# Kernel tuning notes

Measured on AMD Instinct MI355X. Metric: run time of the kernel, lower is better.

Reference implementation:

```python
import jax, jax.numpy as jnp
import numpy as np

B, NS, NQ = 128, 128, 512
D_IN, D_OUT = 256, 64


def setup_inputs() -> dict:
    key = jax.random.key(0)
    ks = jax.random.split(key, 6)
    return {
        "phi_support": jax.random.normal(ks[0], (B, NS, D_IN), dtype=jnp.float32),
        "y_support": jax.random.normal(ks[1], (B, NS, D_OUT), dtype=jnp.float32),
        "phi_query": jax.random.normal(ks[2], (B, NQ, D_IN), dtype=jnp.float32),
        "y_query": jax.random.normal(ks[3], (B, NQ, D_OUT), dtype=jnp.float32),
        # xavier-uniform-ish params
        "m_prior": jax.random.uniform(ks[4], (D_IN, D_OUT), minval=-1.0, maxval=1.0) * np.sqrt(6.0 / (D_IN + D_OUT)),
        "S_inv_prior_asym": jax.random.uniform(ks[5], (D_IN, D_IN), minval=-1.0, maxval=1.0) * np.sqrt(6.0 / (2 * D_IN)),
        "sig_eps": jnp.array([0.1], dtype=jnp.float32),
    }


def reference(phi_support, y_support, phi_query, y_query, m_prior, S_inv_prior_asym, sig_eps):
    alpha = 1.0
    d_out = m_prior.shape[1]
    # prior precision (symmetric PSD by construction) and natural-param prior mean
    S_inv_prior = alpha * (S_inv_prior_asym @ S_inv_prior_asym.T)          # [D_in, D_in]
    m_prior_nat = S_inv_prior @ m_prior                                     # [D_in, D_out]
    # posterior precision / covariance per task (nobs > 0 branch)
    S_inv = jnp.einsum('bni,bnj->bij', phi_support, phi_support) + S_inv_prior  # [B, D_in, D_in]
    S = jnp.linalg.inv(S_inv)                                               # batched small inverse
    rhs = jnp.einsum('bni,bnk->bik', phi_support, y_support) + m_prior_nat  # [B, D_in, D_out]
    m = S @ rhs                                                             # [B, D_in, D_out]
    # predictive mean and spread
    mu = phi_query @ m                                                      # [B, Q, D_out]
    spread_fac = 1.0 + jnp.einsum('bqi,bij,bqj->bq', phi_query, S, phi_query)  # [B, Q]
    # sig = spread_fac (x) (eye * sig_eps) : diagonal [B, Q, D_out, D_out]
    diag = jnp.eye(d_out, dtype=mu.dtype) * sig_eps                         # [D_out, D_out]
    sig = spread_fac[..., None, None] * diag
    # nll: logdet of diagonal sig + quadratic form with its inverse (diag -> reciprocal)
    logdet = d_out * (jnp.log(spread_fac) + jnp.log(sig_eps))               # [B, Q]
    resid = y_query - mu
    quadf = jnp.sum(resid * resid, axis=-1) / (spread_fac * sig_eps)        # [B, Q]
    nll = logdet.mean() + quadf.mean()
    return mu, sig, nll
```

## Files before the change

kernel.cpp:

```cpp
#include <hip/hip_runtime.h>
#include <math.h>

#define B_T   128
#define NS    128
#define NQ    512
#define DIN   256
#define DOUT  64

#define MU_SIZE  (B_T*NQ*DOUT)
#define SIG_SIZE (B_T*NQ*DOUT*DOUT)
#define NLL_IDX  (MU_SIZE + SIG_SIZE)

__global__ __launch_bounds__(256) void k_prior_sp(const float* __restrict__ A,
                                                  double* __restrict__ Sp) {
    __shared__ float Ai[16][260];
    __shared__ float Aj[16][260];
    int bi = blockIdx.x;
    int i0 = (bi >> 4) << 4;
    int j0 = (bi & 15) << 4;
    int tid = threadIdx.x;
    for (int idx = tid; idx < 16 * 256; idx += 256) {
        int r = idx >> 8, c = idx & 255;
        Ai[r][c] = A[(i0 + r) * 256 + c];
        Aj[r][c] = A[(j0 + r) * 256 + c];
    }
    __syncthreads();
    int r = tid >> 4, c = tid & 15;
    double acc = 0.0;
    for (int k = 0; k < 256; ++k)
        acc += (double)Ai[r][k] * (double)Aj[c][k];
    Sp[(i0 + r) * 256 + (j0 + c)] = acc;
}

__global__ __launch_bounds__(64) void k_prior_mpn(const double* __restrict__ Sp,
                                                  const float* __restrict__ MP,
                                                  double* __restrict__ MPN) {
    int i = blockIdx.x, k = threadIdx.x;
    double acc = 0.0;
    for (int t = 0; t < 256; ++t)
        acc += Sp[i * 256 + t] * (double)MP[t * 64 + k];
    MPN[i * 64 + k] = acc;
}

__global__ __launch_bounds__(256) void k_build_G(const float* __restrict__ PHI,
                                                 const double* __restrict__ Sp,
                                                 double* __restrict__ G) {
    __shared__ float As[128][64];
    __shared__ float Bs[128][64];
    int b = blockIdx.x;
    int by = blockIdx.y;
    int ti = 0;
    while (((ti + 1) * (ti + 2)) / 2 <= by) ti++;
    int tj = by - (ti * (ti + 1)) / 2;
    int i0 = ti * 64, j0 = tj * 64;
    int tid = threadIdx.x;
    const float* Pb = PHI + b * (NS * DIN);
    for (int idx = tid; idx < 128 * 64; idx += 256) {
        int n = idx >> 6, c = idx & 63;
        As[n][c] = Pb[n * 256 + i0 + c];
        Bs[n][c] = Pb[n * 256 + j0 + c];
    }
    __syncthreads();
    int tx = tid & 15, ty = tid >> 4;
    double acc[4][4];
#pragma unroll
    for (int r = 0; r < 4; ++r)
#pragma unroll
        for (int s = 0; s < 4; ++s) acc[r][s] = 0.0;
    for (int n = 0; n < 128; ++n) {
        float a0 = As[n][4 * ty + 0], a1 = As[n][4 * ty + 1];
        float a2 = As[n][4 * ty + 2], a3 = As[n][4 * ty + 3];
        float b0 = Bs[n][4 * tx + 0], b1 = Bs[n][4 * tx + 1];
        float b2 = Bs[n][4 * tx + 2], b3 = Bs[n][4 * tx + 3];
        acc[0][0] += (double)a0 * b0; acc[0][1] += (double)a0 * b1;
        acc[0][2] += (double)a0 * b2; acc[0][3] += (double)a0 * b3;
        acc[1][0] += (double)a1 * b0; acc[1][1] += (double)a1 * b1;
        acc[1][2] += (double)a1 * b2; acc[1][3] += (double)a1 * b3;
        acc[2][0] += (double)a2 * b0; acc[2][1] += (double)a2 * b1;
        acc[2][2] += (double)a2 * b2; acc[2][3] += (double)a2 * b3;
        acc[3][0] += (double)a3 * b0; acc[3][1] += (double)a3 * b1;
        acc[3][2] += (double)a3 * b2; acc[3][3] += (double)a3 * b3;
    }
    double* Gb = G + b * 65536;
#pragma unroll
    for (int r = 0; r < 4; ++r) {
        int i = i0 + 4 * ty + r;
#pragma unroll
        for (int s = 0; s < 4; ++s) {
            int j = j0 + 4 * tx + s;
            Gb[i * 256 + j] = acc[r][s] + Sp[i * 256 + j];
        }
    }
}

__global__ __launch_bounds__(256) void k_build_rhs(const float* __restrict__ PHI,
                                                   const float* __restrict__ Y,
                                                   const double* __restrict__ MPN,
                                                   double* __restrict__ RHS) {
    __shared__ float As[128][64];
    __shared__ float Ys[128][64];
    int b = blockIdx.x, i0 = blockIdx.y * 64, tid = threadIdx.x;
    const float* Pb = PHI + b * (NS * DIN);
    const float* Yb = Y + b * (NS * DOUT);
    for (int idx = tid; idx < 128 * 64; idx += 256) {
        int n = idx >> 6, c = idx & 63;
        As[n][c] = Pb[n * 256 + i0 + c];
        Ys[n][c] = Yb[n * 64 + c];
    }
    __syncthreads();
    int tx = tid & 15, ty = tid >> 4;
    double acc[4][4];
#pragma unroll
    for (int r = 0; r < 4; ++r)
#pragma unroll
        for (int s = 0; s < 4; ++s) acc[r][s] = 0.0;
    for (int n = 0; n < 128; ++n) {
        float a0 = As[n][4 * ty + 0], a1 = As[n][4 * ty + 1];
        float a2 = As[n][4 * ty + 2], a3 = As[n][4 * ty + 3];
        float y0 = Ys[n][4 * tx + 0], y1 = Ys[n][4 * tx + 1];
        float y2 = Ys[n][4 * tx + 2], y3 = Ys[n][4 * tx + 3];
        acc[0][0] += (double)a0 * y0; acc[0][1] += (double)a0 * y1;
        acc[0][2] += (double)a0 * y2; acc[0][3] += (double)a0 * y3;
        acc[1][0] += (double)a1 * y0; acc[1][1] += (double)a1 * y1;
        acc[1][2] += (double)a1 * y2; acc[1][3] += (double)a1 * y3;
        acc[2][0] += (double)a2 * y0; acc[2][1] += (double)a2 * y1;
        acc[2][2] += (double)a2 * y2; acc[2][3] += (double)a2 * y3;
        acc[3][0] += (double)a3 * y0; acc[3][1] += (double)a3 * y1;
        acc[3][2] += (double)a3 * y2; acc[3][3] += (double)a3 * y3;
    }
    double* Rb = RHS + b * 16384;
#pragma unroll
    for (int r = 0; r < 4; ++r) {
        int i = i0 + 4 * ty + r;
#pragma unroll
        for (int s = 0; s < 4; ++s) {
            int kc = 4 * tx + s;
            Rb[i * 64 + kc] = acc[r][s] + MPN[i * 64 + kc];
        }
    }
}

__global__ __launch_bounds__(256) void k_chol(double* __restrict__ G,
                                              double* __restrict__ LT,
                                              double* __restrict__ INVD) {
    __shared__ double P[8][256];
    int b = blockIdx.x, tid = threadIdx.x;
    double* Gb = G + b * 65536;
    double* LTb = LT + b * 65536;
    for (int k0 = 0; k0 < 256; k0 += 8) {
#pragma unroll
        for (int p = 0; p < 8; ++p) P[p][tid] = Gb[tid * 256 + k0 + p];
        __syncthreads();
        for (int p = 0; p < 8; ++p) {
            int k = k0 + p;
            if (tid >= k) {
                double v = P[p][tid];
                for (int p2 = 0; p2 < p; ++p2) v -= P[p2][tid] * P[p2][k];
                P[p][tid] = v;
            }
            __syncthreads();
            double d = sqrt(fmax(P[p][k], 1e-300));
            double inv = 1.0 / d;
            if (tid > k) P[p][tid] *= inv;
            else if (tid == k) { P[p][tid] = d; INVD[b * 256 + k] = inv; }
            __syncthreads();
        }
#pragma unroll
        for (int p = 0; p < 8; ++p) {
            int k = k0 + p;
            if (tid >= k) LTb[k * 256 + tid] = P[p][tid];
        }
        int ty = tid >> 4, tx = tid & 15;
        for (int i = k0 + 8 + ty; i < 256; i += 16) {
            double pi[8];
#pragma unroll
            for (int p = 0; p < 8; ++p) pi[p] = P[p][i];
            for (int j = k0 + 8 + tx; j <= i; j += 16) {
                double g = Gb[i * 256 + j];
#pragma unroll
                for (int p = 0; p < 8; ++p) g -= pi[p] * P[p][j];
                Gb[i * 256 + j] = g;
            }
        }
        __syncthreads();
    }
}

__global__ __launch_bounds__(256) void k_trinv(const double* __restrict__ LT,
                                               double* __restrict__ TI,
                                               float* __restrict__ TIF) {
    __shared__ double SHD[8192];
    int b = blockIdx.x, tid = threadIdx.x;
    const double* LTb = LT + b * 65536;
    double* TIb = TI + b * 65536;
    float* TIFb = TIF + b * 65536;
    for (int idx = tid; idx < 65536; idx += 256) {
        int i = idx >> 8, k = idx & 255;
        if (k > i) { TIb[idx] = 0.0; TIFb[idx] = 0.0f; }
    }
    for (int idx = tid; idx < 8192; idx += 256) {
        int g = idx >> 10, rem = idx & 1023, k = rem >> 5, i = rem & 31;
        SHD[idx] = LTb[(32 * g + k) * 256 + 32 * g + i];
    }
    __syncthreads();
    {
        int g = tid >> 5, j = tid & 31;
        const double* D = SHD + g * 1024;
        double x[32];
#pragma unroll
        for (int i = 0; i < 32; ++i) {
            double s = (i == j) ? 1.0 : 0.0;
#pragma unroll
            for (int k = 0; k < i; ++k) {
                double lv = D[k * 32 + i];
                s -= (k >= j) ? lv * x[k] : 0.0;
            }
            double inv = 1.0 / D[i * 32 + i];
            x[i] = (i >= j) ? s * inv : 0.0;
        }
#pragma unroll
        for (int i = 0; i < 32; ++i) {
            int gi = 32 * g + i, gj = 32 * g + j;
            TIb[gi * 256 + gj] = x[i];
            TIFb[gi * 256 + gj] = (float)x[i];
        }
    }
    __syncthreads();
    double* Bsh = SHD;
    int j = tid & 31, ig = tid >> 5;
    for (int I = 1; I < 8; ++I) {
        for (int J = I - 1; J >= 0; --J) {
            double acc[4] = {0.0, 0.0, 0.0, 0.0};
            for (int K = J; K < I; ++K) {
                for (int kk = 0; kk < 32; ++kk) {
                    double tv = TIb[(32 * K + kk) * 256 + 32 * J + j];
#pragma unroll
                    for (int r = 0; r < 4; ++r) {
                        double lv = LTb[(32 * K + kk) * 256 + 32 * I + ig * 4 + r];
                        acc[r] += lv * tv;
                    }
                }
            }
            __syncthreads();
#pragma unroll
            for (int r = 0; r < 4; ++r) Bsh[(ig * 4 + r) * 32 + j] = acc[r];
            __syncthreads();
            double c[4] = {0.0, 0.0, 0.0, 0.0};
            for (int k = 0; k < 32; ++k) {
                double bv = Bsh[k * 32 + j];
#pragma unroll
                for (int r = 0; r < 4; ++r) {
                    double dv = TIb[(32 * I + ig * 4 + r) * 256 + 32 * I + k];
                    c[r] -= dv * bv;
                }
            }
#pragma unroll
            for (int r = 0; r < 4; ++r) {
                int gi = 32 * I + ig * 4 + r, gj = 32 * J + j;
                TIb[gi * 256 + gj] = c[r];
                TIFb[gi * 256 + gj] = (float)c[r];
            }
        }
        __syncthreads();
    }
}

__global__ __launch_bounds__(256) void k_gemm_Z(const double* __restrict__ TI,
                                                const double* __restrict__ RHS,
                                                double* __restrict__ Z) {
    __shared__ double As[32][64];
    __shared__ double Bs[64][64];
    int b = blockIdx.x, i0 = blockIdx.y * 32;
    int tid = threadIdx.x, c = tid & 63, rg = tid >> 6;
    const double* TIb = TI + b * 65536;
    const double* Rb = RHS + b * 16384;
    double* Zb = Z + b * 16384;
    double acc[8] = {};
    for (int k0 = 0; k0 <= i0; k0 += 64) {
        for (int idx = tid; idx < 2048; idx += 256) {
            int r = idx >> 6, kk = idx & 63;
            As[r][kk] = TIb[(i0 + r) * 256 + k0 + kk];
        }
        for (int idx = tid; idx < 4096; idx += 256) {
            int kk = idx >> 6, cc = idx & 63;
            Bs[kk][cc] = Rb[(k0 + kk) * 64 + cc];
        }
        __syncthreads();
        for (int kk = 0; kk < 64; ++kk) {
            double bv = Bs[kk][c];
#pragma unroll
            for (int r = 0; r < 8; ++r)
                acc[r] += As[rg * 8 + r][kk] * bv;
        }
        __syncthreads();
    }
#pragma unroll
    for (int r = 0; r < 8; ++r)
        Zb[(i0 + rg * 8 + r) * 64 + c] = acc[r];
}

__global__ __launch_bounds__(256) void k_gemm_M(const double* __restrict__ TI,
                                                const double* __restrict__ Z,
                                                double* __restrict__ M) {
    __shared__ double As[64][32];
    __shared__ double Bs[64][64];
    int b = blockIdx.x, i0 = blockIdx.y * 32;
    int tid = threadIdx.x, c = tid & 63, rg = tid >> 6;
    const double* TIb = TI + b * 65536;
    const double* Zb = Z + b * 16384;
    double* Mb = M + b * 16384;
    double acc[8] = {};
    for (int k0 = (i0 >> 6) << 6; k0 < 256; k0 += 64) {
        for (int idx = tid; idx < 2048; idx += 256) {
            int kk = idx >> 5, ri = idx & 31;
            As[kk][ri] = TIb[(k0 + kk) * 256 + i0 + ri];
        }
        for (int idx = tid; idx < 4096; idx += 256) {
            int kk = idx >> 6, cc = idx & 63;
            Bs[kk][cc] = Zb[(k0 + kk) * 64 + cc];
        }
        __syncthreads();
        for (int kk = 0; kk < 64; ++kk) {
            double bv = Bs[kk][c];
#pragma unroll
            for (int r = 0; r < 8; ++r)
                acc[r] += As[kk][rg * 8 + r] * bv;
        }
        __syncthreads();
    }
#pragma unroll
    for (int r = 0; r < 8; ++r)
        Mb[(i0 + rg * 8 + r) * 64 + c] = acc[r];
}

__global__ __launch_bounds__(256) void k_spread_gemm(const float* __restrict__ PHIQ,
                                                     const float* __restrict__ TIF,
                                                     float* __restrict__ PSUM) {
    __shared__ float Qs[64][65];
    __shared__ float Ts[64][65];
    int b = blockIdx.x, q0 = blockIdx.y * 64, I = blockIdx.z, i0 = I * 64;
    int tid = threadIdx.x, tx = tid & 15, ty = tid >> 4;
    const float* Qb = PHIQ + b * (NQ * DIN) + q0 * DIN;
    const float* Tb = TIF + b * 65536;
    float acc[4][4];
#pragma unroll
    for (int r = 0; r < 4; ++r)
#pragma unroll
        for (int s = 0; s < 4; ++s) acc[r][s] = 0.0f;
    for (int k0 = 0; k0 <= i0; k0 += 64) {
        for (int idx = tid; idx < 4096; idx += 256) {
            int r = idx >> 6, c = idx & 63;
            Qs[r][c] = Qb[r * 256 + k0 + c];
            Ts[c][r] = Tb[(i0 + r) * 256 + k0 + c];
        }
        __syncthreads();
        for (int kk = 0; kk < 64; ++kk) {
            float a0 = Qs[4 * ty + 0][kk], a1 = Qs[4 * ty + 1][kk];
            float a2 = Qs[4 * ty + 2][kk], a3 = Qs[4 * ty + 3][kk];
            float b0 = Ts[kk][4 * tx + 0], b1 = Ts[kk][4 * tx + 1];
            float b2 = Ts[kk][4 * tx + 2], b3 = Ts[kk][4 * tx + 3];
            acc[0][0] += a0 * b0; acc[0][1] += a0 * b1; acc[0][2] += a0 * b2; acc[0][3] += a0 * b3;
            acc[1][0] += a1 * b0; acc[1][1] += a1 * b1; acc[1][2] += a1 * b2; acc[1][3] += a1 * b3;
            acc[2][0] += a2 * b0; acc[2][1] += a2 * b1; acc[2][2] += a2 * b2; acc[2][3] += a2 * b3;
            acc[3][0] += a3 * b0; acc[3][1] += a3 * b1; acc[3][2] += a3 * b2; acc[3][3] += a3 * b3;
        }
        __syncthreads();
    }
#pragma unroll
    for (int r = 0; r < 4; ++r) {
        float p = acc[r][0] * acc[r][0] + acc[r][1] * acc[r][1]
                + acc[r][2] * acc[r][2] + acc[r][3] * acc[r][3];
        p += __shfl_down(p, 8, 16);
        p += __shfl_down(p, 4, 16);
        p += __shfl_down(p, 2, 16);
        p += __shfl_down(p, 1, 16);
        if (tx == 0) PSUM[(size_t)(b * 4 + I) * 512 + q0 + 4 * ty + r] = p;
    }
}

__global__ __launch_bounds__(256) void k_spread_combine(const float* __restrict__ PSUM,
                                                        float* __restrict__ SPREAD) {
    int b = blockIdx.x;
    for (int q = threadIdx.x; q < 512; q += 256) {
        float s = 1.0f;
#pragma unroll
        for (int I = 0; I < 4; ++I) s += PSUM[(size_t)(b * 4 + I) * 512 + q];
        SPREAD[b * 512 + q] = s;
    }
}

__global__ __launch_bounds__(256) void k_mu(const float* __restrict__ PHIQ,
                                            const double* __restrict__ M,
                                            float* __restrict__ MU) {
    __shared__ float Qs[64][65];
    __shared__ float Ms[64][64];
    int b = blockIdx.x, q0 = blockIdx.y * 64, tid = threadIdx.x;
    int tx = tid & 15, ty = tid >> 4;
    const float* Qb = PHIQ + b * (NQ * DIN) + q0 * DIN;
    const double* Mb = M + b * 16384;
    float acc[4][4];
#pragma unroll
    for (int r = 0; r < 4; ++r)
#pragma unroll
        for (int s = 0; s < 4; ++s) acc[r][s] = 0.0f;
    for (int c0 = 0; c0 < 256; c0 += 64) {
        for (int idx = tid; idx < 4096; idx += 256) {
            int r = idx >> 6, c = idx & 63;
            Qs[r][c] = Qb[r * 256 + c0 + c];
            Ms[r][c] = (float)Mb[(c0 + r) * 64 + c];
        }
        __syncthreads();
        for (int kk = 0; kk < 64; ++kk) {
            float a0 = Qs[4 * ty + 0][kk], a1 = Qs[4 * ty + 1][kk];
            float a2 = Qs[4 * ty + 2][kk], a3 = Qs[4 * ty + 3][kk];
            float b0 = Ms[kk][4 * tx + 0], b1 = Ms[kk][4 * tx + 1];
            float b2 = Ms[kk][4 * tx + 2], b3 = Ms[kk][4 * tx + 3];
            acc[0][0] += a0 * b0; acc[0][1] += a0 * b1; acc[0][2] += a0 * b2; acc[0][3] += a0 * b3;
            acc[1][0] += a1 * b0; acc[1][1] += a1 * b1; acc[1][2] += a1 * b2; acc[1][3] += a1 * b3;
            acc[2][0] += a2 * b0; acc[2][1] += a2 * b1; acc[2][2] += a2 * b2; acc[2][3] += a2 * b3;
            acc[3][0] += a3 * b0; acc[3][1] += a3 * b1; acc[3][2] += a3 * b2; acc[3][3] += a3 * b3;
        }
        __syncthreads();
    }
#pragma unroll
    for (int r = 0; r < 4; ++r) {
        float4 v = make_float4(acc[r][0], acc[r][1], acc[r][2], acc[r][3]);
        *(float4*)&MU[(b * NQ + q0 + 4 * ty + r) * 64 + 4 * tx] = v;
    }
}

__global__ __launch_bounds__(256) void k_nll_part(const float* __restrict__ YQ,
                                                  const float* __restrict__ MU,
                                                  const float* __restrict__ SPREAD,
                                                  const float* __restrict__ SE,
                                                  double* __restrict__ NLLP) {
    __shared__ double red[256];
    int tid = threadIdx.x;
    int bq = blockIdx.x * 256 + tid;
    float se = SE[0];
    float sp = SPREAD[bq];
    float qs = 0.0f;
    const float4* y4 = (const float4*)(YQ + bq * 64);
    const float4* m4 = (const float4*)(MU + bq * 64);
#pragma unroll
    for (int t = 0; t < 16; ++t) {
        float4 y = y4[t], m = m4[t];
        float dx = y.x - m.x, dy = y.y - m.y, dz = y.z - m.z, dw = y.w - m.w;
        qs += dx * dx + dy * dy + dz * dz + dw * dw;
    }
    float val = 64.0f * (logf(sp) + logf(se)) + qs / (sp * se);
    red[tid] = (double)val;
    __syncthreads();
    for (int s = 128; s > 0; s >>= 1) {
        if (tid < s) red[tid] += red[tid + s];
        __syncthreads();
    }
    if (tid == 0) NLLP[blockIdx.x] = red[0] * (1.0 / 65536.0);
}

__global__ __launch_bounds__(256) void k_nll_final(const double* __restrict__ NLLP,
                                                   float* __restrict__ out) {
    __shared__ double red[256];
    int tid = threadIdx.x;
    red[tid] = NLLP[tid];
    __syncthreads();
    for (int s = 128; s > 0; s >>= 1) {
        if (tid < s) red[tid] += red[tid + s];
        __syncthreads();
    }
    if (tid == 0) out[NLL_IDX] = (float)red[0];
}

__global__ __launch_bounds__(256) void k_sig(const float* __restrict__ SPREAD,
                                             const float* __restrict__ SE,
                                             float* __restrict__ out) {
    __shared__ float sv_s;
    int bq = blockIdx.x, tid = threadIdx.x;
    if (tid == 0) sv_s = SPREAD[bq] * SE[0];
    __syncthreads();
    float sv = sv_s;
    float* base = out + (size_t)MU_SIZE + (size_t)bq * 4096;
    int i = tid >> 2;
    int jb = (tid & 3) << 4;
    int d = i - jb;
    float vals[16];
#pragma unroll
    for (int t = 0; t < 16; ++t) vals[t] = (t == d) ? sv : 0.0f;
    float4* p = (float4*)(base + tid * 16);
    p[0] = make_float4(vals[0], vals[1], vals[2], vals[3]);
    p[1] = make_float4(vals[4], vals[5], vals[6], vals[7]);
    p[2] = make_float4(vals[8], vals[9], vals[10], vals[11]);
    p[3] = make_float4(vals[12], vals[13], vals[14], vals[15]);
}

extern "C" void kernel_launch(void* const* d_in, const int* in_sizes, int n_in,
                              void* d_out, int out_size, void* d_ws, size_t ws_size,
                              hipStream_t stream) {
    const float* PHI_S = (const float*)d_in[0];
    const float* Y_S   = (const float*)d_in[1];
    const float* PHI_Q = (const float*)d_in[2];
    const float* Y_Q   = (const float*)d_in[3];
    const float* MP    = (const float*)d_in[4];
    const float* AP    = (const float*)d_in[5];
    const float* SE    = (const float*)d_in[6];
    float* out = (float*)d_out;

    double* scratch = (double*)(out + MU_SIZE);
    double* G    = scratch;
    double* LT   = G + 8388608;
    double* RHS  = LT + 8388608;
    double* Z    = RHS + 2097152;
    double* TI   = Z + 2097152;
    double* Spd  = TI + 8388608;
    double* MPN  = Spd + 65536;
    double* INVD = MPN + 16384;
    float*  TIF  = (float*)(INVD + 32768);
    float*  PSUM = TIF + 8388608;
    float*  SPREAD = (float*)d_ws;
    double* NLLP   = (double*)((char*)d_ws + 65536 * 4);

    k_prior_sp      <<<256, 256, 0, stream>>>(AP, Spd);
    k_prior_mpn     <<<256, 64, 0, stream>>>(Spd, MP, MPN);
    k_build_G       <<<dim3(B_T, 10), 256, 0, stream>>>(PHI_S, Spd, G);
    k_build_rhs     <<<dim3(B_T, 4), 256, 0, stream>>>(PHI_S, Y_S, MPN, RHS);
    k_chol          <<<B_T, 256, 0, stream>>>(G, LT, INVD);
    k_trinv         <<<B_T, 256, 0, stream>>>(LT, TI, TIF);
    k_gemm_Z        <<<dim3(B_T, 8), 256, 0, stream>>>(TI, RHS, Z);
    k_gemm_M        <<<dim3(B_T, 8), 256, 0, stream>>>(TI, Z, RHS);
    k_spread_gemm   <<<dim3(B_T, 8, 4), 256, 0, stream>>>(PHI_Q, TIF, PSUM);
    k_spread_combine<<<B_T, 256, 0, stream>>>(PSUM, SPREAD);
    k_mu            <<<dim3(B_T, 8), 256, 0, stream>>>(PHI_Q, RHS, out);
    k_nll_part      <<<256, 256, 0, stream>>>(Y_Q, out, SPREAD, SE, NLLP);
    k_nll_final     <<<1, 256, 0, stream>>>(NLLP, out);
    k_sig           <<<65536, 256, 0, stream>>>(SPREAD, SE, out);
}
```

Baseline: 2.502 ms.

## Widen Cholesky panels to 32 with wavefront factorization; transpose Q tiles for float4 LDS reads

The blocked Cholesky now uses 32-column panels instead of 8. The diagonal block is factored inside one wavefront using shuffles, the panel rows below are solved per thread, and the trailing update is done in 2-column register tiles, with a skewed LDS index to avoid bank conflicts. This cuts the number of block-wide barriers and the passes over G in global memory, but leaves most threads idle during the diagonal factorization and adds register pressure (32-element arrays). Separately, the spread and mu GEMMs store the Q tile transposed so each thread can read its A operand with a single float4 LDS load.

```diff
diff --git a/kernel.cpp b/kernel.cpp
--- a/kernel.cpp
+++ b/kernel.cpp
@@ -140,46 +140,75 @@
     }
 }
 
+#define PP(p, row) P[p][((row) + (p)) & 255]
+
 __global__ __launch_bounds__(256) void k_chol(double* __restrict__ G,
-                                              double* __restrict__ LT,
-                                              double* __restrict__ INVD) {
-    __shared__ double P[8][256];
+                                              double* __restrict__ LT) {
+    __shared__ double P[32][256];
+    __shared__ double dinvs[32];
     int b = blockIdx.x, tid = threadIdx.x;
     double* Gb = G + b * 65536;
     double* LTb = LT + b * 65536;
-    for (int k0 = 0; k0 < 256; k0 += 8) {
-#pragma unroll
-        for (int p = 0; p < 8; ++p) P[p][tid] = Gb[tid * 256 + k0 + p];
-        __syncthreads();
-        for (int p = 0; p < 8; ++p) {
-            int k = k0 + p;
-            if (tid >= k) {
-                double v = P[p][tid];
-                for (int p2 = 0; p2 < p; ++p2) v -= P[p2][tid] * P[p2][k];
-                P[p][tid] = v;
-            }
-            __syncthreads();
-            double d = sqrt(fmax(P[p][k], 1e-300));
-            double inv = 1.0 / d;
-            if (tid > k) P[p][tid] *= inv;
-            else if (tid == k) { P[p][tid] = d; INVD[b * 256 + k] = inv; }
-            __syncthreads();
-        }
-#pragma unroll
-        for (int p = 0; p < 8; ++p) {
-            int k = k0 + p;
-            if (tid >= k) LTb[k * 256 + tid] = P[p][tid];
+    for (int k0 = 0; k0 < 256; k0 += 32) {
+        int rows = 256 - k0;
+        for (int idx = tid; idx < rows * 32; idx += 256) {
+            int r = k0 + (idx >> 5), p = idx & 31;
+            PP(p, r) = Gb[r * 256 + k0 + p];
+        }
+        __syncthreads();
+        if (tid < 32) {
+            double x[32];
+#pragma unroll
+            for (int p = 0; p < 32; ++p) x[p] = PP(p, k0 + tid);
+            for (int p = 0; p < 32; ++p) {
+                double dpp = __shfl(x[p], p);
+                double d = sqrt(fmax(dpp, 1e-300));
+                double inv = 1.0 / d;
+                if (tid == p) { x[p] = d; dinvs[p] = inv; }
+                else if (tid > p) x[p] *= inv;
+                for (int p2 = p + 1; p2 < 32; ++p2) {
+                    double lp2 = __shfl(x[p], p2);
+                    if (tid >= p2) x[p2] -= x[p] * lp2;
+                }
+            }
+#pragma unroll
+            for (int p = 0; p < 32; ++p) PP(p, k0 + tid) = x[p];
+        }
+        __syncthreads();
+        if (tid >= k0 + 32) {
+            int i = tid;
+            double xr[32];
+#pragma unroll
+            for (int p = 0; p < 32; ++p) {
+                double v = PP(p, i);
+                for (int p2 = 0; p2 < p; ++p2)
+                    v -= xr[p2] * PP(p2, k0 + p);
+                xr[p] = v * dinvs[p];
+            }
+#pragma unroll
+            for (int p = 0; p < 32; ++p) PP(p, i) = xr[p];
+        }
+        __syncthreads();
+        for (int p = 0; p < 32; ++p) {
+            int r = k0 + p + tid;
+            if (r < 256) LTb[(k0 + p) * 256 + r] = PP(p, r);
         }
         int ty = tid >> 4, tx = tid & 15;
-        for (int i = k0 + 8 + ty; i < 256; i += 16) {
-            double pi[8];
-#pragma unroll
-            for (int p = 0; p < 8; ++p) pi[p] = P[p][i];
-            for (int j = k0 + 8 + tx; j <= i; j += 16) {
-                double g = Gb[i * 256 + j];
-#pragma unroll
-                for (int p = 0; p < 8; ++p) g -= pi[p] * P[p][j];
-                Gb[i * 256 + j] = g;
+        for (int i = k0 + 32 + ty; i < 256; i += 16) {
+            double pi[32];
+#pragma unroll
+            for (int p = 0; p < 32; ++p) pi[p] = PP(p, i);
+            for (int jg = k0 + 32; jg <= i; jg += 32) {
+                int j = jg + 2 * tx;
+                double g0 = Gb[i * 256 + j];
+                double g1 = Gb[i * 256 + j + 1];
+#pragma unroll
+                for (int p = 0; p < 32; ++p) {
+                    g0 -= pi[p] * PP(p, j);
+                    g1 -= pi[p] * PP(p, j + 1);
+                }
+                if (j <= i) Gb[i * 256 + j] = g0;
+                if (j + 1 <= i) Gb[i * 256 + j + 1] = g1;
             }
         }
         __syncthreads();
@@ -336,8 +365,8 @@
 __global__ __launch_bounds__(256) void k_spread_gemm(const float* __restrict__ PHIQ,
                                                      const float* __restrict__ TIF,
                                                      float* __restrict__ PSUM) {
-    __shared__ float Qs[64][65];
-    __shared__ float Ts[64][65];
+    __shared__ float Qs[64][68];
+    __shared__ float Ts[64][68];
     int b = blockIdx.x, q0 = blockIdx.y * 64, I = blockIdx.z, i0 = I * 64;
     int tid = threadIdx.x, tx = tid & 15, ty = tid >> 4;
     const float* Qb = PHIQ + b * (NQ * DIN) + q0 * DIN;
@@ -350,19 +379,17 @@
     for (int k0 = 0; k0 <= i0; k0 += 64) {
         for (int idx = tid; idx < 4096; idx += 256) {
             int r = idx >> 6, c = idx & 63;
-            Qs[r][c] = Qb[r * 256 + k0 + c];
+            Qs[c][r] = Qb[r * 256 + k0 + c];
             Ts[c][r] = Tb[(i0 + r) * 256 + k0 + c];
         }
         __syncthreads();
         for (int kk = 0; kk < 64; ++kk) {
-            float a0 = Qs[4 * ty + 0][kk], a1 = Qs[4 * ty + 1][kk];
-            float a2 = Qs[4 * ty + 2][kk], a3 = Qs[4 * ty + 3][kk];
-            float b0 = Ts[kk][4 * tx + 0], b1 = Ts[kk][4 * tx + 1];
-            float b2 = Ts[kk][4 * tx + 2], b3 = Ts[kk][4 * tx + 3];
-            acc[0][0] += a0 * b0; acc[0][1] += a0 * b1; acc[0][2] += a0 * b2; acc[0][3] += a0 * b3;
-            acc[1][0] += a1 * b0; acc[1][1] += a1 * b1; acc[1][2] += a1 * b2; acc[1][3] += a1 * b3;
-            acc[2][0] += a2 * b0; acc[2][1] += a2 * b1; acc[2][2] += a2 * b2; acc[2][3] += a2 * b3;
-            acc[3][0] += a3 * b0; acc[3][1] += a3 * b1; acc[3][2] += a3 * b2; acc[3][3] += a3 * b3;
+            float4 a = *(const float4*)&Qs[kk][4 * ty];
+            float4 bb = *(const float4*)&Ts[kk][4 * tx];
+            acc[0][0] += a.x * bb.x; acc[0][1] += a.x * bb.y; acc[0][2] += a.x * bb.z; acc[0][3] += a.x * bb.w;
+            acc[1][0] += a.y * bb.x; acc[1][1] += a.y * bb.y; acc[1][2] += a.y * bb.z; acc[1][3] += a.y * bb.w;
+            acc[2][0] += a.z * bb.x; acc[2][1] += a.z * bb.y; acc[2][2] += a.z * bb.z; acc[2][3] += a.z * bb.w;
+            acc[3][0] += a.w * bb.x; acc[3][1] += a.w * bb.y; acc[3][2] += a.w * bb.z; acc[3][3] += a.w * bb.w;
         }
         __syncthreads();
     }
@@ -392,7 +419,7 @@
 __global__ __launch_bounds__(256) void k_mu(const float* __restrict__ PHIQ,
                                             const double* __restrict__ M,
                                             float* __restrict__ MU) {
-    __shared__ float Qs[64][65];
+    __shared__ float Qs[64][68];
     __shared__ float Ms[64][64];
     int b = blockIdx.x, q0 = blockIdx.y * 64, tid = threadIdx.x;
     int tx = tid & 15, ty = tid >> 4;
@@ -406,19 +433,17 @@
     for (int c0 = 0; c0 < 256; c0 += 64) {
         for (int idx = tid; idx < 4096; idx += 256) {
             int r = idx >> 6, c = idx & 63;
-            Qs[r][c] = Qb[r * 256 + c0 + c];
+            Qs[c][r] = Qb[r * 256 + c0 + c];
             Ms[r][c] = (float)Mb[(c0 + r) * 64 + c];
         }
         __syncthreads();
         for (int kk = 0; kk < 64; ++kk) {
-            float a0 = Qs[4 * ty + 0][kk], a1 = Qs[4 * ty + 1][kk];
-            float a2 = Qs[4 * ty + 2][kk], a3 = Qs[4 * ty + 3][kk];
-            float b0 = Ms[kk][4 * tx + 0], b1 = Ms[kk][4 * tx + 1];
-            float b2 = Ms[kk][4 * tx + 2], b3 = Ms[kk][4 * tx + 3];
-            acc[0][0] += a0 * b0; acc[0][1] += a0 * b1; acc[0][2] += a0 * b2; acc[0][3] += a0 * b3;
-            acc[1][0] += a1 * b0; acc[1][1] += a1 * b1; acc[1][2] += a1 * b2; acc[1][3] += a1 * b3;
-            acc[2][0] += a2 * b0; acc[2][1] += a2 * b1; acc[2][2] += a2 * b2; acc[2][3] += a2 * b3;
-            acc[3][0] += a3 * b0; acc[3][1] += a3 * b1; acc[3][2] += a3 * b2; acc[3][3] += a3 * b3;
+            float4 a = *(const float4*)&Qs[kk][4 * ty];
+            float4 bb = *(const float4*)&Ms[kk][4 * tx];
+            acc[0][0] += a.x * bb.x; acc[0][1] += a.x * bb.y; acc[0][2] += a.x * bb.z; acc[0][3] += a.x * bb.w;
+            acc[1][0] += a.y * bb.x; acc[1][1] += a.y * bb.y; acc[1][2] += a.y * bb.z; acc[1][3] += a.y * bb.w;
+            acc[2][0] += a.z * bb.x; acc[2][1] += a.z * bb.y; acc[2][2] += a.z * bb.z; acc[2][3] += a.z * bb.w;
+            acc[3][0] += a.w * bb.x; acc[3][1] += a.w * bb.y; acc[3][2] += a.w * bb.z; acc[3][3] += a.w * bb.w;
         }
         __syncthreads();
     }
@@ -513,8 +538,7 @@
     double* TI   = Z + 2097152;
     double* Spd  = TI + 8388608;
     double* MPN  = Spd + 65536;
-    double* INVD = MPN + 16384;
-    float*  TIF  = (float*)(INVD + 32768);
+    float*  TIF  = (float*)(MPN + 16384);
     float*  PSUM = TIF + 8388608;
     float*  SPREAD = (float*)d_ws;
     double* NLLP   = (double*)((char*)d_ws + 65536 * 4);
@@ -523,7 +547,7 @@
     k_prior_mpn     <<<256, 64, 0, stream>>>(Spd, MP, MPN);
     k_build_G       <<<dim3(B_T, 10), 256, 0, stream>>>(PHI_S, Spd, G);
     k_build_rhs     <<<dim3(B_T, 4), 256, 0, stream>>>(PHI_S, Y_S, MPN, RHS);
-    k_chol          <<<B_T, 256, 0, stream>>>(G, LT, INVD);
+    k_chol          <<<B_T, 256, 0, stream>>>(G, LT);
     k_trinv         <<<B_T, 256, 0, stream>>>(LT, TI, TIF);
     k_gemm_Z        <<<dim3(B_T, 8), 256, 0, stream>>>(TI, RHS, Z);
     k_gemm_M        <<<dim3(B_T, 8), 256, 0, stream>>>(TI, Z, RHS);
```

Result: slower. 3.264 ms (+30.4%).
